# Kernel tuning notes

Hardware: AMD Instinct MI355X
Metric: run time of the kernel (lower is better)

Reference implementation:

```python
import jax, jax.numpy as jnp
import numpy as np


def _conv2d(x, w, pad):
    return jax.lax.conv_general_dilated(
        x, w, (1, 1), [(pad, pad), (pad, pad)],
        dimension_numbers=('NCHW', 'OIHW', 'NCHW'))


def _affine_grid(theta, k):
    # torch F.affine_grid, align_corners=False; output size (k, k)
    base = ((2.0 * jnp.arange(k) + 1.0) / k - 1.0).astype(jnp.float32)
    pts = jnp.stack([
        jnp.broadcast_to(base[None, :], (k, k)),  # x varies along width
        jnp.broadcast_to(base[:, None], (k, k)),  # y varies along height
        jnp.ones((k, k), jnp.float32)], -1)        # [k,k,3]
    return jnp.einsum('ijc,nrc->nijr', pts, theta)  # [N,k,k,2] -> (x,y)


def _grid_sample(img, grid):
    # torch F.grid_sample: bilinear, zeros padding, align_corners=False
    # img [C,H,W], grid [k,k,2] with (x,y) in [-1,1]
    C, H, W = img.shape
    gx = (grid[..., 0] + 1.0) * W * 0.5 - 0.5
    gy = (grid[..., 1] + 1.0) * H * 0.5 - 0.5
    x0 = jnp.floor(gx); y0 = jnp.floor(gy)
    wx = gx - x0; wy = gy - y0
    x0i = x0.astype(jnp.int32); y0i = y0.astype(jnp.int32)

    def gath(yi, xi):
        valid = ((xi >= 0) & (xi < W) & (yi >= 0) & (yi < H)).astype(img.dtype)
        v = img[:, jnp.clip(yi, 0, H - 1), jnp.clip(xi, 0, W - 1)]  # [C,k,k]
        return v * valid[None]

    v00 = gath(y0i, x0i); v01 = gath(y0i, x0i + 1)
    v10 = gath(y0i + 1, x0i); v11 = gath(y0i + 1, x0i + 1)
    return (v00 * ((1 - wx) * (1 - wy))[None] + v01 * (wx * (1 - wy))[None]
            + v10 * ((1 - wx) * wy)[None] + v11 * (wx * wy)[None])


def reference(x, stn0_w, stn0_b, stn1_w, lin_w, lin_b, check):
    B, C, H, W = x.shape
    k = stn1_w.shape[-1]
    h = jax.nn.relu(_conv2d(x, stn0_w, k // 2) + stn0_b[None, :, None, None])
    ident6 = jnp.array([1., 0., 0., 0., 1., 0.], jnp.float32)
    out = _conv2d(h, stn1_w, 0) * (1.0 - check) + ident6[None, :, None, None]
    Ho, Wo = out.shape[2], out.shape[3]
    N = B * Ho * Wo
    # permute(0,3,2,1).view(N,2,3) as in torch
    theta = out.transpose(0, 3, 2, 1).reshape(N, 2, 3)
    grid = _affine_grid(theta, k)  # [N,k,k,2]
    xv = jnp.arange(k // 2, k // 2 + Ho, dtype=jnp.float32)[:, None]  # meshgrid 'ij'
    yv = jnp.arange(k // 2, k // 2 + Wo, dtype=jnp.float32)[None, :]
    half = float(k // 2)
    auxx = ((grid[..., 0] * half).reshape(B, Ho, Wo, k, k)
            + xv[None, :, :, None, None]).reshape(N, k, k) / (H - 1) * 2.0 - 1.0
    auxy = ((grid[..., 1] * half).reshape(B, Ho, Wo, k, k)
            + yv[None, :, :, None, None]).reshape(N, k, k) / (W - 1) * 2.0 - 1.0
    auxgrid = jnp.stack([auxx, auxy], -1).reshape(B, Ho * Wo, k, k, 2)
    # tile(x,0,Ho*Wo) duplicates x[b] for each of its Ho*Wo grids; gather directly
    xs = jax.vmap(lambda img, g: jax.vmap(lambda gg: _grid_sample(img, gg))(g))(x, auxgrid)  # [B,P,C,k,k]
    x_out = xs.reshape(N, -1) @ lin_w.T + lin_b  # [N,O]
    score = x_out.reshape(B, Ho, Wo, -1).transpose(0, 3, 2, 1)  # [B,O,Wo,Ho] as in torch
    ident23 = jnp.array([[1., 0., 0.], [0., 1., 0.]], jnp.float32)
    return score, ident23[None] - theta, out, auxx, auxy


def setup_inputs() -> dict:
    key = jax.random.key(0)
    ks = jax.random.split(key, 6)
    C, O, k = 128, 256, 3
    B, H, W = 8, 56, 56
    x = jax.random.normal(ks[0], (B, C, H, W), jnp.float32)
    stn0_w = jax.random.normal(ks[1], (C, C, k, k), jnp.float32) * (1.0 / np.sqrt(C * k * k))
    stn0_b = jax.random.normal(ks[2], (C,), jnp.float32) * 0.01
    # original zero-inits stn1; use small random so theta is non-trivial
    stn1_w = jax.random.normal(ks[3], (6, C, k, k), jnp.float32) * 0.01
    lin_w = jax.random.normal(ks[4], (O, C * k * k), jnp.float32) * (1.0 / np.sqrt(C * k * k))
    lin_b = jax.random.normal(ks[5], (O,), jnp.float32) * 0.01
    return {'x': x, 'stn0_w': stn0_w, 'stn0_b': stn0_b, 'stn1_w': stn1_w,
            'lin_w': lin_w, 'lin_b': lin_b, 'check': 0}
```

## Files before the change

kernel.cpp:

```cpp
#include <hip/hip_runtime.h>

typedef __attribute__((ext_vector_type(4))) float f32x4;
typedef __attribute__((ext_vector_type(8))) short bf16x8;

#define OPLANE 2916
#define NN 23328
#define KDIM 1152
#define PLANE 3136
#define LDP 72
#define BS_LDP 1160

__device__ __forceinline__ unsigned short f2bf(float f) {
    unsigned u = __builtin_bit_cast(unsigned, f);
    u += 0x7fffu + ((u >> 16) & 1u);
    return (unsigned short)(u >> 16);
}
__device__ __forceinline__ float bflo(unsigned u) {
    return __builtin_bit_cast(float, u << 16);
}
__device__ __forceinline__ float bfhi(unsigned u) {
    return __builtin_bit_cast(float, u & 0xffff0000u);
}

__global__ __launch_bounds__(256) void k_pre(const float* __restrict__ x,
                                             const float* __restrict__ w0,
                                             const float* __restrict__ lw,
                                             const float* __restrict__ w1,
                                             unsigned short* __restrict__ xnh,
                                             unsigned short* __restrict__ b1t,
                                             unsigned short* __restrict__ b2t,
                                             unsigned short* __restrict__ b3t) {
    __shared__ unsigned short lds[56 * 132];
    if (blockIdx.x < 1728) {
        int idx = blockIdx.x * 256 + threadIdx.x;
        if (idx < 147456) {
            int r = idx / KDIM, k = idx - r * KDIM;
            int ij = k >> 7, ic = k & 127;
            b1t[idx] = f2bf(w0[r * KDIM + ic * 9 + ij]);
        } else {
            int j = idx - 147456;
            int r = j / KDIM, k = j - r * KDIM;
            int ij = k >> 7, ic = k & 127;
            b2t[j] = f2bf(lw[r * KDIM + ic * 9 + ij]);
        }
    } else if (blockIdx.x < 1800) {
        int idx = (blockIdx.x - 1728) * 256 + threadIdx.x;
        int r = idx / KDIM, k = idx - r * KDIM;
        int ij = k >> 7, ic = k & 127;
        b3t[idx] = (r < 6) ? f2bf(w1[r * KDIM + ic * 9 + ij]) : (unsigned short)0;
    } else {
        const int bid = blockIdx.x - 1800;
        const int y = bid % 56, b = bid / 56, tid = threadIdx.x;
        for (int i = tid; i < 7168; i += 256) {
            int ic = i / 56, xc = i - ic * 56;
            lds[xc * 132 + ic] = f2bf(x[(b * 128 + ic) * PLANE + y * 56 + xc]);
        }
        __syncthreads();
        for (int i = tid; i < 7168; i += 256) {
            int xc = i >> 7, ic = i & 127;
            xnh[(b * PLANE + y * 56 + xc) * 128 + ic] = lds[xc * 132 + ic];
        }
    }
}

__global__ __launch_bounds__(512) void k_gemm1(const unsigned short* __restrict__ xnh,
                                               const unsigned short* __restrict__ Bt,
                                               const float* __restrict__ bias,
                                               unsigned short* __restrict__ h) {
    __shared__ unsigned short As[2][64 * LDP];
    __shared__ unsigned short Bs[2][128 * LDP];
    const int tid = threadIdx.x;
    const int lane = tid & 63, wid = tid >> 6;
    const int wr = wid >> 2, wc = wid & 3;
    const int mt_id = (blockIdx.x & 7) * 49 + (blockIdx.x >> 3);
    const int m0 = mt_id * 64;

    f32x4 acc[2][2];
    #pragma unroll
    for (int mt = 0; mt < 2; mt++)
        #pragma unroll
        for (int nt = 0; nt < 2; nt++) { acc[mt][nt][0]=0.f; acc[mt][nt][1]=0.f; acc[mt][nt][2]=0.f; acc[mt][nt][3]=0.f; }

    const int row = tid >> 3, q = tid & 7;
    const int p = m0 + row;
    const int b = p / PLANE; int rem = p - b * PLANE;
    const int y = rem / 56; const int xc = rem - y * 56;
    const int aswo = row * LDP + q * 8;
    const int brow = tid >> 2, bq = tid & 3;
    const unsigned short* bg = Bt + brow * KDIM + bq * 16;
    const int bswo = brow * LDP + bq * 16;
    const int lm = lane & 15, lq = lane >> 4;

    uint4 a0, bv0, bv1;
    auto issue = [&](int it) {
        const int ij = it >> 1;
        const int di = ij / 3, dj = ij - di * 3;
        const int icb = (it & 1) << 6;
        a0 = make_uint4(0u,0u,0u,0u);
        bool valid = (y + di >= 1) && (y + di <= 56) && (xc + dj >= 1) && (xc + dj <= 56);
        if (valid) {
            const unsigned short* ap = xnh + (p + (di - 1) * 56 + (dj - 1)) * 128 + icb + q * 8;
            a0 = *(const uint4*)ap;
        }
        bv0 = *(const uint4*)(bg + it * 64);
        bv1 = *(const uint4*)(bg + it * 64 + 8);
    };

    issue(0);
    *(uint4*)(&As[0][aswo]) = a0;
    *(uint4*)(&Bs[0][bswo + 0]) = bv0;
    *(uint4*)(&Bs[0][bswo + 8]) = bv1;
    __syncthreads();

    #pragma unroll
    for (int it = 0; it < 18; it++) {
        const int cur = it & 1;
        if (it < 17) issue(it + 1);
        #pragma unroll
        for (int kk = 0; kk < 64; kk += 32) {
            bf16x8 af[2], bf[2];
            #pragma unroll
            for (int mt = 0; mt < 2; mt++)
                af[mt] = *(const bf16x8*)&As[cur][(wr * 32 + mt * 16 + lm) * LDP + kk + lq * 8];
            #pragma unroll
            for (int nt = 0; nt < 2; nt++)
                bf[nt] = *(const bf16x8*)&Bs[cur][(wc * 32 + nt * 16 + lm) * LDP + kk + lq * 8];
            #pragma unroll
            for (int mt = 0; mt < 2; mt++)
                #pragma unroll
                for (int nt = 0; nt < 2; nt++)
                    acc[mt][nt] = __builtin_amdgcn_mfma_f32_16x16x32_bf16(af[mt], bf[nt], acc[mt][nt], 0, 0, 0);
        }
        if (it < 17) {
            const int nxt = cur ^ 1;
            *(uint4*)(&As[nxt][aswo]) = a0;
            *(uint4*)(&Bs[nxt][bswo + 0]) = bv0;
            *(uint4*)(&Bs[nxt][bswo + 8]) = bv1;
            __syncthreads();
        }
    }
    #pragma unroll
    for (int mt = 0; mt < 2; mt++) {
        int m = m0 + wr * 32 + mt * 16 + lq * 4;
        #pragma unroll
        for (int nt = 0; nt < 2; nt++) {
            int n = wc * 32 + nt * 16 + lm;
            float bb = bias[n];
            #pragma unroll
            for (int r = 0; r < 4; r++)
                h[(m + r) * 128 + n] = f2bf(fmaxf(acc[mt][nt][r] + bb, 0.f));
        }
    }
}

__global__ __launch_bounds__(256) void k_conv2f(const unsigned short* __restrict__ h,
                                                const unsigned short* __restrict__ Wt2,
                                                const int* __restrict__ check,
                                                float* __restrict__ o_out,
                                                float* __restrict__ o_th,
                                                float* __restrict__ o_ax,
                                                float* __restrict__ o_ay,
                                                float* __restrict__ sxy) {
    __shared__ unsigned short Bs[16 * BS_LDP];
    __shared__ unsigned short As[64 * LDP];
    __shared__ float vals[64 * 6];
    const int bid = (blockIdx.x & 7) * 46 + (blockIdx.x >> 3);
    if (bid >= 365) return;
    const int tid = threadIdx.x;
    const int lane = tid & 63, wid = tid >> 6;
    const int lm = lane & 15, lq = lane >> 4;
    const int m0 = bid * 64;

    {
        const int r = tid >> 4, kb = (tid & 15) * 72;
        const unsigned short* src = Wt2 + r * KDIM + kb;
        unsigned short* dst = &Bs[r * BS_LDP + kb];
        #pragma unroll
        for (int jj = 0; jj < 9; jj++)
            *(uint4*)(dst + jj * 8) = *(const uint4*)(src + jj * 8);
    }

    const int row = tid >> 2, q = tid & 3;
    const int p = min(m0 + row, NN - 1);
    const int b = p / OPLANE; const int rr = p - b * OPLANE;
    const int oh = rr / 54, ow = rr - oh * 54;
    const int hbase = b * PLANE + oh * 56 + ow;
    unsigned short* asw = &As[row * LDP + q * 16];

    f32x4 acc; acc[0] = 0.f; acc[1] = 0.f; acc[2] = 0.f; acc[3] = 0.f;

    uint4 a0, a1;
    auto issue = [&](int it) {
        const int ij = it >> 1;
        const int di = ij / 3, dj = ij - di * 3;
        const int icb = (it & 1) << 6;
        const unsigned short* ap = h + (hbase + di * 56 + dj) * 128 + icb + q * 16;
        a0 = *(const uint4*)ap;
        a1 = *(const uint4*)(ap + 8);
    };
    issue(0);

    #pragma unroll
    for (int it = 0; it < 18; it++) {
        __syncthreads();
        *(uint4*)(asw + 0) = a0;
        *(uint4*)(asw + 8) = a1;
        __syncthreads();
        if (it < 17) issue(it + 1);
        #pragma unroll
        for (int kk = 0; kk < 64; kk += 32) {
            bf16x8 af = *(const bf16x8*)&As[(wid * 16 + lm) * LDP + kk + lq * 8];
            bf16x8 bf = *(const bf16x8*)&Bs[lm * BS_LDP + it * 64 + kk + lq * 8];
            acc = __builtin_amdgcn_mfma_f32_16x16x32_bf16(af, bf, acc, 0, 0, 0);
        }
    }

    if (lm < 6) {
        #pragma unroll
        for (int r4 = 0; r4 < 4; r4++)
            vals[(wid * 16 + lq * 4 + r4) * 6 + lm] = acc[r4];
    }
    __syncthreads();

    if (tid < 64) {
        int p2 = m0 + tid;
        if (p2 < NN) {
            int b2 = p2 / OPLANE; int r2 = p2 - b2 * OPLANE;
            int oh2 = r2 / 54; int ow2 = r2 - oh2 * 54;
            float val[6];
            float s = 1.0f - (float)check[0];
            const float id6[6] = {1.f, 0.f, 0.f, 0.f, 1.f, 0.f};
            #pragma unroll
            for (int r = 0; r < 6; r++) val[r] = vals[tid * 6 + r] * s + id6[r];
            int n = (b2 * 54 + ow2) * 54 + oh2;
            #pragma unroll
            for (int r = 0; r < 6; r++) {
                o_out[((b2 * 6 + r) * 54 + oh2) * 54 + ow2] = val[r];
                o_th[n * 6 + r] = id6[r] - val[r];
            }
            const float bse[3] = {-2.f / 3.f, 0.f, 2.f / 3.f};
            #pragma unroll
            for (int i = 0; i < 3; i++)
                #pragma unroll
                for (int j = 0; j < 3; j++) {
                    float gx = bse[j] * val[0] + bse[i] * val[1] + val[2];
                    float gy = bse[j] * val[3] + bse[i] * val[4] + val[5];
                    float ax = (gx + 1.f + (float)ow2) * (2.f / 55.f) - 1.f;
                    float ay = (gy + 1.f + (float)oh2) * (2.f / 55.f) - 1.f;
                    int ij = i * 3 + j;
                    o_ax[n * 9 + ij] = ax;
                    o_ay[n * 9 + ij] = ay;
                    sxy[(n * 9 + ij) * 2 + 0] = (ax + 1.f) * 28.f - 0.5f;
                    sxy[(n * 9 + ij) * 2 + 1] = (ay + 1.f) * 28.f - 0.5f;
                }
        }
    }
}

__global__ __launch_bounds__(256) void k_sgemm(const unsigned short* __restrict__ xnh,
                                               const unsigned short* __restrict__ Wt,
                                               const float* __restrict__ bias,
                                               const float* __restrict__ sxy,
                                               float* __restrict__ score) {
    __shared__ unsigned short Ss[64 * LDP];
    __shared__ unsigned short Ws[128 * LDP];
    const int i = blockIdx.x;
    const int xcd = i & 7, j = i >> 3;
    const int pp = xcd * 46 + (j >> 1);
    const int m8 = j & 1;
    if (pp >= 365) return;
    const int o0 = m8 * 128;
    const int s0 = pp * 64;
    const int tid = threadIdx.x;
    const int lane = tid & 63, wid = tid >> 6;
    const int wr = wid >> 1, wc = wid & 1;

    f32x4 acc[4][2];
    #pragma unroll
    for (int mt = 0; mt < 4; mt++)
        #pragma unroll
        for (int nt = 0; nt < 2; nt++) { acc[mt][nt][0]=0.f; acc[mt][nt][1]=0.f; acc[mt][nt][2]=0.f; acc[mt][nt][3]=0.f; }

    const int row = tid >> 2, q = tid & 3;
    const int mp = min(s0 + row, NN - 1);
    const int b = mp / OPLANE; const int rr = mp - b * OPLANE;
    const int ho = rr / 54, wo = rr - (rr / 54) * 54;
    const int n = (b * 54 + wo) * 54 + ho;
    const int xbase = b * PLANE;
    unsigned short* ssw = &Ss[row * LDP + q * 16];
    const int wrow = tid >> 1, wq = tid & 1;
    const unsigned short* wg = Wt + (o0 + wrow) * KDIM + wq * 32;
    unsigned short* wsw = &Ws[wrow * LDP + wq * 32];
    const int lm = lane & 15, lq = lane >> 4;

    float2 sc[9];
    {
        const float* spp = sxy + n * 18;
        #pragma unroll
        for (int ij = 0; ij < 9; ij++) sc[ij] = *(const float2*)(spp + ij * 2);
    }

    int off0 = 0, off1 = 0, off2 = 0, off3 = 0;
    float wt0 = 0.f, wt1 = 0.f, wt2 = 0.f, wt3 = 0.f;
    auto mkoff = [&](int ij) {
        float sx = sc[ij].x, sy = sc[ij].y;
        float x0f = floorf(sx), y0f = floorf(sy);
        float wx = sx - x0f, wy = sy - y0f;
        int x0 = (int)x0f, y0 = (int)y0f;
        int x1 = x0 + 1, y1 = y0 + 1;
        float vx0 = (x0 >= 0 && x0 < 56) ? 1.f : 0.f;
        float vx1 = (x1 >= 0 && x1 < 56) ? 1.f : 0.f;
        float vy0 = (y0 >= 0 && y0 < 56) ? 1.f : 0.f;
        float vy1 = (y1 >= 0 && y1 < 56) ? 1.f : 0.f;
        int xc0 = min(max(x0, 0), 55), xc1 = min(max(x1, 0), 55);
        int yc0 = min(max(y0, 0), 55), yc1 = min(max(y1, 0), 55);
        off0 = (xbase + yc0 * 56 + xc0) << 7;
        off1 = (xbase + yc0 * 56 + xc1) << 7;
        off2 = (xbase + yc1 * 56 + xc0) << 7;
        off3 = (xbase + yc1 * 56 + xc1) << 7;
        wt0 = vy0 * vx0 * (1.f - wx) * (1.f - wy);
        wt1 = vy0 * vx1 * wx * (1.f - wy);
        wt2 = vy1 * vx0 * (1.f - wx) * wy;
        wt3 = vy1 * vx1 * wx * wy;
    };

    uint4 p0a, p0b, p1a, p1b, p2a, p2b, p3a, p3b;
    uint4 w0v, w1v, w2v, w3v;
    auto issue = [&](int it) {
        const int co = ((it & 1) << 6) + q * 16;
        p0a = *(const uint4*)(xnh + off0 + co);
        p0b = *(const uint4*)(xnh + off0 + co + 8);
        p1a = *(const uint4*)(xnh + off1 + co);
        p1b = *(const uint4*)(xnh + off1 + co + 8);
        p2a = *(const uint4*)(xnh + off2 + co);
        p2b = *(const uint4*)(xnh + off2 + co + 8);
        p3a = *(const uint4*)(xnh + off3 + co);
        p3b = *(const uint4*)(xnh + off3 + co + 8);
        w0v = *(const uint4*)(wg + it * 64);
        w1v = *(const uint4*)(wg + it * 64 + 8);
        w2v = *(const uint4*)(wg + it * 64 + 16);
        w3v = *(const uint4*)(wg + it * 64 + 24);
    };

    mkoff(0);
    issue(0);

    #pragma unroll
    for (int it = 0; it < 18; it++) {
        unsigned dw[8];
        const unsigned* d0 = (const unsigned*)&p0a;
        const unsigned* d1 = (const unsigned*)&p1a;
        const unsigned* d2 = (const unsigned*)&p2a;
        const unsigned* d3 = (const unsigned*)&p3a;
        const unsigned* e0 = (const unsigned*)&p0b;
        const unsigned* e1 = (const unsigned*)&p1b;
        const unsigned* e2 = (const unsigned*)&p2b;
        const unsigned* e3 = (const unsigned*)&p3b;
        #pragma unroll
        for (int d = 0; d < 8; d++) {
            unsigned u0 = (d < 4) ? d0[d] : e0[d - 4];
            unsigned u1 = (d < 4) ? d1[d] : e1[d - 4];
            unsigned u2 = (d < 4) ? d2[d] : e2[d - 4];
            unsigned u3 = (d < 4) ? d3[d] : e3[d - 4];
            float lo = wt0 * bflo(u0) + wt1 * bflo(u1) + wt2 * bflo(u2) + wt3 * bflo(u3);
            float hi = wt0 * bfhi(u0) + wt1 * bfhi(u1) + wt2 * bfhi(u2) + wt3 * bfhi(u3);
            unsigned pk;
            asm("v_cvt_pk_bf16_f32 %0, %1, %2" : "=v"(pk) : "v"(lo), "v"(hi));
            dw[d] = pk;
        }
        __syncthreads();
        *(uint4*)(ssw + 0) = *(uint4*)&dw[0];
        *(uint4*)(ssw + 8) = *(uint4*)&dw[4];
        *(uint4*)(wsw + 0)  = w0v;
        *(uint4*)(wsw + 8)  = w1v;
        *(uint4*)(wsw + 16) = w2v;
        *(uint4*)(wsw + 24) = w3v;
        __syncthreads();
        if (it < 17) {
            if (((it + 1) & 1) == 0) mkoff((it + 1) >> 1);
            issue(it + 1);
        }
        #pragma unroll
        for (int kk = 0; kk < 64; kk += 32) {
            bf16x8 wf[4], sf[2];
            #pragma unroll
            for (int mt = 0; mt < 4; mt++)
                wf[mt] = *(const bf16x8*)&Ws[(wr * 64 + mt * 16 + lm) * LDP + kk + lq * 8];
            #pragma unroll
            for (int nt = 0; nt < 2; nt++)
                sf[nt] = *(const bf16x8*)&Ss[(wc * 32 + nt * 16 + lm) * LDP + kk + lq * 8];
            #pragma unroll
            for (int mt = 0; mt < 4; mt++)
                #pragma unroll
                for (int nt = 0; nt < 2; nt++)
                    acc[mt][nt] = __builtin_amdgcn_mfma_f32_16x16x32_bf16(wf[mt], sf[nt], acc[mt][nt], 0, 0, 0);
        }
    }
    #pragma unroll
    for (int mt = 0; mt < 4; mt++) {
        #pragma unroll
        for (int r = 0; r < 4; r++) {
            int o = o0 + wr * 64 + mt * 16 + lq * 4 + r;
            float bb = bias[o];
            #pragma unroll
            for (int nt = 0; nt < 2; nt++) {
                int s = s0 + wc * 32 + nt * 16 + lm;
                if (s < NN) {
                    int sb = s / OPLANE;
                    int soff = s - sb * OPLANE;
                    score[(sb * 256 + o) * OPLANE + soff] = acc[mt][nt][r] + bb;
                }
            }
        }
    }
}

extern "C" void kernel_launch(void* const* d_in, const int* in_sizes, int n_in,
                              void* d_out, int out_size, void* d_ws, size_t ws_size,
                              hipStream_t stream) {
    const float* x  = (const float*)d_in[0];
    const float* w0 = (const float*)d_in[1];
    const float* b0 = (const float*)d_in[2];
    const float* w1 = (const float*)d_in[3];
    const float* lw = (const float*)d_in[4];
    const float* lb = (const float*)d_in[5];
    const int* check = (const int*)d_in[6];

    float* out   = (float*)d_out;
    float* score = out;
    float* o_th  = out + 5971968;
    float* o_out = out + 6111936;
    float* o_ax  = out + 6251904;
    float* o_ay  = out + 6461856;

    char* wsb = (char*)d_ws;
    unsigned short* h   = (unsigned short*)wsb;
    unsigned short* b3t = (unsigned short*)(wsb + 6422528);
    unsigned short* xnh = (unsigned short*)(wsb + 12845056);
    unsigned short* b1t = (unsigned short*)(wsb + 19267584);
    unsigned short* b2t = (unsigned short*)(wsb + 19562496);
    float* sxy = (float*)(wsb + 20152320);

    k_pre<<<2248, 256, 0, stream>>>(x, w0, lw, w1, xnh, b1t, b2t, b3t);
    k_gemm1<<<392, 512, 0, stream>>>(xnh, b1t, b0, h);
    k_conv2f<<<368, 256, 0, stream>>>(h, b3t, check, o_out, o_th, o_ax, o_ay, sxy);
    k_sgemm<<<736, 256, 0, stream>>>(xnh, b2t, lb, sxy, score);
}
```

Baseline: 154.8 us.

## Compute all 256 outputs per sgemm block to avoid duplicate bilinear sampling

The sampling GEMM now uses 512-thread blocks that cover all 256 output channels for a 64-position tile. Before, the output channels were split across two blocks, so the bilinear gather and interpolation ran twice per position. The sampling work per thread is halved and done once per block, and the weight tile in shared memory doubles. Each block now carries more LDS and more threads, which may lower occupancy.

```diff
diff --git a/kernel.cpp b/kernel.cpp
--- a/kernel.cpp
+++ b/kernel.cpp
@@ -257,23 +257,21 @@
     }
 }
 
-__global__ __launch_bounds__(256) void k_sgemm(const unsigned short* __restrict__ xnh,
+__global__ __launch_bounds__(512) void k_sgemm(const unsigned short* __restrict__ xnh,
                                                const unsigned short* __restrict__ Wt,
                                                const float* __restrict__ bias,
                                                const float* __restrict__ sxy,
                                                float* __restrict__ score) {
     __shared__ unsigned short Ss[64 * LDP];
-    __shared__ unsigned short Ws[128 * LDP];
+    __shared__ unsigned short Ws[256 * LDP];
     const int i = blockIdx.x;
-    const int xcd = i & 7, j = i >> 3;
-    const int pp = xcd * 46 + (j >> 1);
-    const int m8 = j & 1;
+    const int pp = (i & 7) * 46 + (i >> 3);
     if (pp >= 365) return;
-    const int o0 = m8 * 128;
     const int s0 = pp * 64;
     const int tid = threadIdx.x;
     const int lane = tid & 63, wid = tid >> 6;
-    const int wr = wid >> 1, wc = wid & 1;
+    const int wr = wid >> 1;
+    const int wc = wid & 1;
 
     f32x4 acc[4][2];
     #pragma unroll
@@ -281,15 +279,15 @@
         #pragma unroll
         for (int nt = 0; nt < 2; nt++) { acc[mt][nt][0]=0.f; acc[mt][nt][1]=0.f; acc[mt][nt][2]=0.f; acc[mt][nt][3]=0.f; }
 
-    const int row = tid >> 2, q = tid & 3;
+    const int row = tid >> 3, q = tid & 7;
     const int mp = min(s0 + row, NN - 1);
     const int b = mp / OPLANE; const int rr = mp - b * OPLANE;
     const int ho = rr / 54, wo = rr - (rr / 54) * 54;
     const int n = (b * 54 + wo) * 54 + ho;
     const int xbase = b * PLANE;
-    unsigned short* ssw = &Ss[row * LDP + q * 16];
+    unsigned short* ssw = &Ss[row * LDP + q * 8];
     const int wrow = tid >> 1, wq = tid & 1;
-    const unsigned short* wg = Wt + (o0 + wrow) * KDIM + wq * 32;
+    const unsigned short* wg = Wt + wrow * KDIM + wq * 32;
     unsigned short* wsw = &Ws[wrow * LDP + wq * 32];
     const int lm = lane & 15, lq = lane >> 4;
 
@@ -324,18 +322,14 @@
         wt3 = vy1 * vx1 * wx * wy;
     };
 
-    uint4 p0a, p0b, p1a, p1b, p2a, p2b, p3a, p3b;
+    uint4 p0, p1, p2, p3;
     uint4 w0v, w1v, w2v, w3v;
     auto issue = [&](int it) {
-        const int co = ((it & 1) << 6) + q * 16;
-        p0a = *(const uint4*)(xnh + off0 + co);
-        p0b = *(const uint4*)(xnh + off0 + co + 8);
-        p1a = *(const uint4*)(xnh + off1 + co);
-        p1b = *(const uint4*)(xnh + off1 + co + 8);
-        p2a = *(const uint4*)(xnh + off2 + co);
-        p2b = *(const uint4*)(xnh + off2 + co + 8);
-        p3a = *(const uint4*)(xnh + off3 + co);
-        p3b = *(const uint4*)(xnh + off3 + co + 8);
+        const int co = ((it & 1) << 6) + q * 8;
+        p0 = *(const uint4*)(xnh + off0 + co);
+        p1 = *(const uint4*)(xnh + off1 + co);
+        p2 = *(const uint4*)(xnh + off2 + co);
+        p3 = *(const uint4*)(xnh + off3 + co);
         w0v = *(const uint4*)(wg + it * 64);
         w1v = *(const uint4*)(wg + it * 64 + 8);
         w2v = *(const uint4*)(wg + it * 64 + 16);
@@ -347,21 +341,14 @@
 
     #pragma unroll
     for (int it = 0; it < 18; it++) {
-        unsigned dw[8];
-        const unsigned* d0 = (const unsigned*)&p0a;
-        const unsigned* d1 = (const unsigned*)&p1a;
-        const unsigned* d2 = (const unsigned*)&p2a;
-        const unsigned* d3 = (const unsigned*)&p3a;
-        const unsigned* e0 = (const unsigned*)&p0b;
-        const unsigned* e1 = (const unsigned*)&p1b;
-        const unsigned* e2 = (const unsigned*)&p2b;
-        const unsigned* e3 = (const unsigned*)&p3b;
-        #pragma unroll
-        for (int d = 0; d < 8; d++) {
-            unsigned u0 = (d < 4) ? d0[d] : e0[d - 4];
-            unsigned u1 = (d < 4) ? d1[d] : e1[d - 4];
-            unsigned u2 = (d < 4) ? d2[d] : e2[d - 4];
-            unsigned u3 = (d < 4) ? d3[d] : e3[d - 4];
+        unsigned dw[4];
+        const unsigned* c0 = (const unsigned*)&p0;
+        const unsigned* c1 = (const unsigned*)&p1;
+        const unsigned* c2 = (const unsigned*)&p2;
+        const unsigned* c3 = (const unsigned*)&p3;
+        #pragma unroll
+        for (int d = 0; d < 4; d++) {
+            unsigned u0 = c0[d], u1 = c1[d], u2 = c2[d], u3 = c3[d];
             float lo = wt0 * bflo(u0) + wt1 * bflo(u1) + wt2 * bflo(u2) + wt3 * bflo(u3);
             float hi = wt0 * bfhi(u0) + wt1 * bfhi(u1) + wt2 * bfhi(u2) + wt3 * bfhi(u3);
             unsigned pk;
@@ -369,8 +356,7 @@
             dw[d] = pk;
         }
         __syncthreads();
-        *(uint4*)(ssw + 0) = *(uint4*)&dw[0];
-        *(uint4*)(ssw + 8) = *(uint4*)&dw[4];
+        *(uint4*)ssw = *(uint4*)dw;
         *(uint4*)(wsw + 0)  = w0v;
         *(uint4*)(wsw + 8)  = w1v;
         *(uint4*)(wsw + 16) = w2v;
@@ -400,7 +386,7 @@
     for (int mt = 0; mt < 4; mt++) {
         #pragma unroll
         for (int r = 0; r < 4; r++) {
-            int o = o0 + wr * 64 + mt * 16 + lq * 4 + r;
+            int o = wr * 64 + mt * 16 + lq * 4 + r;
             float bb = bias[o];
             #pragma unroll
             for (int nt = 0; nt < 2; nt++) {
@@ -444,5 +430,5 @@
     k_pre<<<2248, 256, 0, stream>>>(x, w0, lw, w1, xnh, b1t, b2t, b3t);
     k_gemm1<<<392, 512, 0, stream>>>(xnh, b1t, b0, h);
     k_conv2f<<<368, 256, 0, stream>>>(h, b3t, check, o_out, o_th, o_ax, o_ay, sxy);
-    k_sgemm<<<736, 256, 0, stream>>>(xnh, b2t, lb, sxy, score);
-}
+    k_sgemm<<<368, 512, 0, stream>>>(xnh, b2t, lb, sxy, score);
+}
```

After: 158.3 us. 1.02x slower.
